# Performance work log

Measured on AMD Instinct MI355X. Metric: run time of the kernel, lower is better.

The kernel has to match this reference:

```python
import jax, jax.numpy as jnp
import numpy as np

BS, L, D, K, G, E = 512, 128, 512, 30, 8, 2048
H = E // 2  # MLP hidden = embed_dim // 2


def setup_inputs():
    key = jax.random.key(0)
    ks = jax.random.split(key, 8)
    features = jax.random.normal(ks[0], (BS, L, D), jnp.float32)
    atten = jax.random.uniform(ks[1], (BS, L, L), jnp.float32)
    rng = np.random.default_rng(0)
    lens = rng.integers(34, L - 1, size=BS)          # caption lengths (>= 34 so lengths-2 > K)
    toks = rng.integers(1, 1000, size=(BS, L))
    pos = np.arange(L)[None, :]
    text = np.where(pos < lens[:, None], toks, 0)    # zero padding
    text[np.arange(BS), lens - 1] = 49407            # eos = max token id -> argmax finds it
    text = jnp.asarray(text, jnp.int32)
    pid = jnp.asarray(np.repeat(np.arange(BS // G), G), jnp.int32)  # 64 groups of size G=8
    dlp_w = jax.random.normal(ks[2], (G, D), jnp.float32)           # weights['weight_8']
    dlp_b = jnp.zeros((G,), jnp.float32)                            # biases['bias_8']
    dlp_lw = jax.random.normal(ks[3], (K * G, E), jnp.float32) * 0.05  # linears['linear_8']
    dlp_lb = jnp.zeros((E,), jnp.float32)
    mlp_w1 = jax.random.normal(ks[4], (D, H), jnp.float32) * 0.04
    mlp_b1 = jnp.zeros((H,), jnp.float32)
    bn_g = jnp.ones((H,), jnp.float32)
    bn_b = jnp.zeros((H,), jnp.float32)
    mlp_w2 = jax.random.normal(ks[5], (H, E), jnp.float32) * 0.03
    mlp_b2 = jnp.zeros((E,), jnp.float32)
    return dict(features=features, atten=atten, text=text, pid=pid,
                dlp_w=dlp_w, dlp_b=dlp_b, dlp_lw=dlp_lw, dlp_lb=dlp_lb,
                mlp_w1=mlp_w1, mlp_b1=mlp_b1, bn_g=bn_g, bn_b=bn_b,
                mlp_w2=mlp_w2, mlp_b2=mlp_b2)


def _l2norm(x, eps=1e-8):
    return x / (jnp.sqrt(jnp.sum(x * x, axis=-1, keepdims=True)) + eps)


def _groups_from_pid(pid_np):
    # replicates the pid_dist==0 grouping + dedup-by-member-set, preserving first-seen order
    groups, order = {}, []
    for i, p in enumerate(pid_np.tolist()):
        if p not in groups:
            groups[p] = []
            order.append(p)
        groups[p].append(i)
    return [groups[p] for p in order]


def reference(features, atten, text, pid, dlp_w, dlp_b, dlp_lw, dlp_lb,
              mlp_w1, mlp_b1, bn_g, bn_b, mlp_w2, mlp_b2):
    bs = features.shape[0]
    b = jnp.arange(bs)
    mask = (text != 0).astype(features.dtype)                  # [bs, L]
    lengths = mask.sum(1) - 2.0                                # [bs]
    eos = jnp.argmax(text, axis=-1)                            # [bs]
    att = atten.at[b, :, eos].set(-1.0).at[:, :, 0].set(-1.0)
    row = att[b, eos, :] * mask                                # [bs, L]
    idx = jax.lax.top_k(row, K)[1]                             # [bs, K] topk token indices
    feats = jnp.take_along_axis(features, idx[:, :, None], axis=1)  # [bs, K, D]

    # pid-based dynamic grouping (host-side; pid is an index input, static)
    glists = _groups_from_pid(np.asarray(pid))
    assert {len(g) for g in glists} == {G}, 'expert params provided for group size G only'
    gi = np.asarray(glists)                                    # [ng, G]
    xg = feats[gi].reshape(gi.shape[0], G * K, D)              # concat group members: [ng, G*K, D]
    # F.linear(x, W[G,D], b).T  ->  [ng, G, G*K]
    h = jnp.einsum('ntd,gd->ngt', xg, dlp_w) + dlp_b[None, :, None]
    yg = h @ dlp_lw + dlp_lb                                   # linear_G: [ng, G, E]
    # scatter-combine each member's row back to its batch position
    new_base = jnp.zeros((bs, E), feats.dtype).at[gi.reshape(-1)].set(yg.reshape(-1, E))
    new_base = _l2norm(new_base)

    # MLP (Linear -> BatchNorm1d(train stats) -> ReLU -> Linear) on l2-normed gathered feats
    x = _l2norm(feats).reshape(bs * K, D) @ mlp_w1 + mlp_b1
    mu, var = x.mean(0), x.var(0)
    x = jax.nn.relu((x - mu) / jnp.sqrt(var + 1e-5) * bn_g + bn_b)
    x = (x @ mlp_w2 + mlp_b2).reshape(bs, K, E)

    # maxk_pool1d_var with pool k=1: per-channel max over first min(length, K) rows
    lens = jnp.minimum(lengths, K).astype(jnp.int32)
    valid = jnp.arange(K)[None, :] < lens[:, None]             # [bs, K]
    pooled = jnp.max(jnp.where(valid[:, :, None], x, -jnp.inf), axis=1)  # [bs, E]
    return (pooled + new_base).astype(jnp.float32)
```

## Files before the change

kernel.cpp:

```cpp
#include <hip/hip_runtime.h>
#include <hip/hip_bf16.h>

#define BS 512
#define LL 128
#define DD 512
#define KK 30
#define GG 8
#define EE 2048
#define HH 1024
#define NROWS (BS*KK)
#define NG (BS/GG)

typedef __attribute__((ext_vector_type(8))) short bf16x8;
typedef __attribute__((ext_vector_type(4))) float f32x4;
typedef __attribute__((address_space(1))) const unsigned int gu32;
typedef __attribute__((address_space(3))) unsigned int lu32;

__device__ __forceinline__ unsigned short f2bf(float f){
  unsigned int x = __float_as_uint(f);
  x = (x + 0x7FFFu + ((x >> 16) & 1u)) >> 16;
  return (unsigned short)x;
}
__device__ __forceinline__ float bf2f(unsigned short u){
  return __uint_as_float(((unsigned int)u) << 16);
}
__device__ __forceinline__ unsigned fkey(float f){
  unsigned b = __float_as_uint(f);
  return (b & 0x80000000u) ? ~b : (b | 0x80000000u);
}
__device__ __forceinline__ float fdec(unsigned k){
  unsigned b = (k & 0x80000000u) ? (k & 0x7FFFFFFFu) : ~k;
  return __uint_as_float(b);
}

__global__ __launch_bounds__(64) void k_prep(const float* __restrict__ atten,
                                             const int* __restrict__ text,
                                             int* __restrict__ idx,
                                             int* __restrict__ lensk){
  const int b = blockIdx.x;
  const int lane = threadIdx.x;
  const int t0 = text[b*LL + lane];
  const int t1 = text[b*LL + 64 + lane];

  int v, vi;
  if(t1 > t0){ v = t1; vi = lane + 64; } else { v = t0; vi = lane; }
#pragma unroll
  for(int off = 32; off; off >>= 1){
    const int ov = __shfl_xor(v, off), oi = __shfl_xor(vi, off);
    if(ov > v || (ov == v && oi < vi)){ v = ov; vi = oi; }
  }
  const int eos = vi;

  const unsigned long long mb0 = __ballot(t0 != 0), mb1 = __ballot(t1 != 0);
  if(lane == 0) lensk[b] = min(__popcll(mb0) + __popcll(mb1) - 2, KK);

  const float a0 = atten[(size_t)b*LL*LL + (size_t)eos*LL + lane];
  const float a1 = atten[(size_t)b*LL*LL + (size_t)eos*LL + 64 + lane];
  float r0 = (t0 == 0) ? 0.f : ((lane == 0 || lane == eos) ? -1.f : a0);
  float r1 = (t1 == 0) ? 0.f : ((lane + 64 == eos) ? -1.f : a1);

  for(int k = 0; k < KK; k++){
    float mv; int mi;
    if(r1 > r0){ mv = r1; mi = lane + 64; } else { mv = r0; mi = lane; }
#pragma unroll
    for(int off = 32; off; off >>= 1){
      const float ov = __shfl_xor(mv, off); const int oi = __shfl_xor(mi, off);
      if(ov > mv || (ov == mv && oi < mi)){ mv = ov; mi = oi; }
    }
    if(lane == 0) idx[b*KK + k] = mi;
    if(mi == lane)      r0 = -3.f;
    if(mi == lane + 64) r1 = -3.f;
  }
}

__global__ __launch_bounds__(128) void k_gather(const float* __restrict__ features,
                                                const float* __restrict__ dlp_w,
                                                const float* __restrict__ dlp_b,
                                                const int* __restrict__ idx,
                                                unsigned short* __restrict__ nfeats,
                                                float* __restrict__ hval){
  const int r = blockIdx.x;
  const int b = r / KK;
  const int t = threadIdx.x;
  const int l = idx[r];

  const float4 v = ((const float4*)features)[((size_t)b*LL + l)*(DD/4) + t];
  float ss = v.x*v.x + v.y*v.y + v.z*v.z + v.w*v.w;
  float hg[GG];
#pragma unroll
  for(int g = 0; g < GG; g++){
    const float4 w = ((const float4*)dlp_w)[g*(DD/4) + t];
    hg[g] = v.x*w.x + v.y*w.y + v.z*w.z + v.w*w.w;
  }
#pragma unroll
  for(int off = 32; off > 0; off >>= 1){
    ss += __shfl_down(ss, off);
#pragma unroll
    for(int g = 0; g < GG; g++) hg[g] += __shfl_down(hg[g], off);
  }
  __shared__ float red[2][9];
  __shared__ float s_rn;
  const int wave = t >> 6, lane = t & 63;
  if(lane == 0){
    red[wave][0] = ss;
#pragma unroll
    for(int g = 0; g < GG; g++) red[wave][1+g] = hg[g];
  }
  __syncthreads();
  if(t == 0) s_rn = 1.0f / (sqrtf(red[0][0] + red[1][0]) + 1e-8f);
  if(t < GG) hval[(size_t)r*GG + t] = red[0][1+t] + red[1][1+t] + dlp_b[t];
  __syncthreads();
  const float rn = s_rn;
  ushort4 u;
  u.x = f2bf(v.x*rn); u.y = f2bf(v.y*rn); u.z = f2bf(v.z*rn); u.w = f2bf(v.w*rn);
  ((ushort4*)nfeats)[(size_t)r*(DD/4) + t] = u;
}

__global__ __launch_bounds__(256) void k_dlp(const float* __restrict__ hval,
                                             const float* __restrict__ dlp_lw,
                                             const float* __restrict__ dlp_lb,
                                             unsigned short* __restrict__ nbbf){
  const int et = blockIdx.x;
  const int n  = blockIdx.y;
  const int tid = threadIdx.x;
  __shared__ float hs[GG][GG*KK];
  for(int i = tid; i < GG*GG*KK; i += 256){
    const int g = i / (GG*KK), tt = i % (GG*KK);
    const int m = tt / KK, kq = tt % KK;
    hs[g][tt] = hval[(size_t)(((n*GG + m)*KK) + kq)*GG + g];
  }
  __syncthreads();
  const int h = tid >> 7, c = tid & 127;
  const int e = et*128 + c;
  float acc[4] = {0.f, 0.f, 0.f, 0.f};
#pragma unroll 4
  for(int k = 0; k < GG*KK; k++){
    const float w = dlp_lw[(size_t)k*EE + e];
#pragma unroll
    for(int rr = 0; rr < 4; rr++) acc[rr] += hs[h*4 + rr][k] * w;
  }
  const float lb = dlp_lb[e];
#pragma unroll
  for(int rr = 0; rr < 4; rr++)
    nbbf[(size_t)(n*GG + h*4 + rr)*EE + e] = f2bf(acc[rr] + lb);
}

__global__ __launch_bounds__(256) void k_l2nb(unsigned short* __restrict__ nbbf){
  const int b = blockIdx.x, t = threadIdx.x;
  uint4* p = (uint4*)(nbbf + (size_t)b*EE);
  uint4 u = p[t];
  unsigned short* us = (unsigned short*)&u;
  float f[8]; float ss = 0.f;
#pragma unroll
  for(int j = 0; j < 8; j++){ f[j] = bf2f(us[j]); ss += f[j]*f[j]; }
#pragma unroll
  for(int off = 32; off > 0; off >>= 1) ss += __shfl_down(ss, off);
  __shared__ float red[4];
  __shared__ float s_rn;
  if((t & 63) == 0) red[t >> 6] = ss;
  __syncthreads();
  if(t == 0) s_rn = 1.0f / (sqrtf(red[0] + red[1] + red[2] + red[3]) + 1e-8f);
  __syncthreads();
  const float rn = s_rn;
#pragma unroll
  for(int j = 0; j < 8; j++) us[j] = f2bf(f[j]*rn);
  p[t] = u;
}

__global__ __launch_bounds__(256) void k_wcvt(const float* __restrict__ src,
                                              unsigned short* __restrict__ dst,
                                              int Kd, int Nd){
  __shared__ float tile[32][33];
  const int n0 = blockIdx.x*32, k0 = blockIdx.y*32;
  const int r = threadIdx.x >> 3, c4 = (threadIdx.x & 7)*4;
  const float4 v = *(const float4*)(src + (size_t)(k0 + r)*Nd + n0 + c4);
  tile[r][c4+0] = v.x; tile[r][c4+1] = v.y; tile[r][c4+2] = v.z; tile[r][c4+3] = v.w;
  __syncthreads();
  ushort4 u;
  u.x = f2bf(tile[c4+0][r]); u.y = f2bf(tile[c4+1][r]);
  u.z = f2bf(tile[c4+2][r]); u.w = f2bf(tile[c4+3][r]);
  *(ushort4*)(dst + (size_t)(n0 + r)*Kd + k0 + c4) = u;
}

template<int KD, int ND, bool POOL, bool STATS, int NBX>
__global__ __launch_bounds__(512, 2) void k_mgemm(const unsigned short* __restrict__ A,
                                                  const unsigned short* __restrict__ Bt,
                                                  const float* __restrict__ bias,
                                                  unsigned short* __restrict__ obf,
                                                  const int* __restrict__ lensk,
                                                  unsigned* __restrict__ pkey,
                                                  float* __restrict__ psum,
                                                  float* __restrict__ psq){
  __shared__ short S[2][2][256*64];
  const int tid  = threadIdx.x;
  const int wave = tid >> 6, lane = tid & 63;
  const int wr = wave >> 2, wc = wave & 3;
  const int lrow = lane & 15, kg = lane >> 4;

  const int nwg = gridDim.x, cpx = nwg >> 3;
  const int bid = (blockIdx.x & 7)*cpx + (blockIdx.x >> 3);
  const int bx = bid % NBX, by = bid / NBX;
  const int m0 = by*256, n0 = bx*256;

  const unsigned short* Ab = A  + (size_t)m0*KD;
  const unsigned short* Bb = Bt + (size_t)n0*KD;

#define STG_A(tt, p, c) { \
  const int i_ = tid + (c)*512; const int r_ = i_ >> 3; \
  const int g_ = (i_ & 7) ^ (r_ & 7); \
  __builtin_amdgcn_global_load_lds((gu32*)(Ab + (size_t)r_*KD + (tt)*64 + g_*8), \
                                   (lu32*)(&S[p][0][i_*8]), 16, 0, 0); }
#define STG_B(tt, p, c) { \
  const int i_ = tid + (c)*512; const int r_ = i_ >> 3; \
  const int g_ = (i_ & 7) ^ (r_ & 7); \
  __builtin_amdgcn_global_load_lds((gu32*)(Bb + (size_t)r_*KD + (tt)*64 + g_*8), \
                                   (lu32*)(&S[p][1][i_*8]), 16, 0, 0); }

  f32x4 acc[8][4] = {};
  const int NT = KD/64;

  STG_A(0, 0, 0) STG_A(0, 0, 2)
  STG_B(0, 0, 0) STG_B(0, 0, 1) STG_B(0, 0, 2) STG_B(0, 0, 3)
  STG_A(0, 0, 1) STG_A(0, 0, 3)

  const int arow = wr*128 + lrow;
  const int brow = wc*64  + lrow;
  const int gx0 = ((0*4 + kg) ^ (lrow & 7))*8;
  const int gx1 = ((1*4 + kg) ^ (lrow & 7))*8;

  for(int t = 0; t < NT; t++){
    const int p = t & 1;
    const short* Abuf = &S[p][0][0];
    const short* Bbuf = &S[p][1][0];

    asm volatile("s_waitcnt vmcnt(2)" ::: "memory");
    __builtin_amdgcn_s_barrier();
    asm volatile("" ::: "memory");
    if(t + 1 < NT){
      STG_A(t+1, p^1, 0) STG_A(t+1, p^1, 2)
      STG_B(t+1, p^1, 0) STG_B(t+1, p^1, 1) STG_B(t+1, p^1, 2) STG_B(t+1, p^1, 3)
    }
    bf16x8 bg0[4], bg1[4], af[4];
#pragma unroll
    for(int n = 0; n < 4; n++){
      bg0[n] = *(const bf16x8*)(Bbuf + (brow + n*16)*64 + gx0);
      bg1[n] = *(const bf16x8*)(Bbuf + (brow + n*16)*64 + gx1);
    }
#pragma unroll
    for(int m = 0; m < 4; m++)
      af[m] = *(const bf16x8*)(Abuf + (arow + m*16)*64 + gx0);
    __builtin_amdgcn_s_setprio(1);
#pragma unroll
    for(int m = 0; m < 4; m++)
#pragma unroll
      for(int n = 0; n < 4; n++)
        acc[m][n] = __builtin_amdgcn_mfma_f32_16x16x32_bf16(af[m], bg0[n], acc[m][n], 0, 0, 0);
#pragma unroll
    for(int m = 0; m < 4; m++)
      af[m] = *(const bf16x8*)(Abuf + (arow + m*16)*64 + gx1);
#pragma unroll
    for(int m = 0; m < 4; m++)
#pragma unroll
      for(int n = 0; n < 4; n++)
        acc[m][n] = __builtin_amdgcn_mfma_f32_16x16x32_bf16(af[m], bg1[n], acc[m][n], 0, 0, 0);
    __builtin_amdgcn_s_setprio(0);

    if(t + 1 < NT) asm volatile("s_waitcnt vmcnt(6)" ::: "memory");
    else           asm volatile("s_waitcnt vmcnt(0)" ::: "memory");
    __builtin_amdgcn_s_barrier();
    asm volatile("" ::: "memory");
    if(t + 1 < NT){ STG_A(t+1, p^1, 1) STG_A(t+1, p^1, 3) }
#pragma unroll
    for(int m = 0; m < 4; m++)
      af[m] = *(const bf16x8*)(Abuf + (arow + 64 + m*16)*64 + gx0);
    __builtin_amdgcn_s_setprio(1);
#pragma unroll
    for(int m = 0; m < 4; m++)
#pragma unroll
      for(int n = 0; n < 4; n++)
        acc[4+m][n] = __builtin_amdgcn_mfma_f32_16x16x32_bf16(af[m], bg0[n], acc[4+m][n], 0, 0, 0);
#pragma unroll
    for(int m = 0; m < 4; m++)
      af[m] = *(const bf16x8*)(Abuf + (arow + 64 + m*16)*64 + gx1);
#pragma unroll
    for(int m = 0; m < 4; m++)
#pragma unroll
      for(int n = 0; n < 4; n++)
        acc[4+m][n] = __builtin_amdgcn_mfma_f32_16x16x32_bf16(af[m], bg1[n], acc[4+m][n], 0, 0, 0);
    __builtin_amdgcn_s_setprio(0);
  }
#undef STG_A
#undef STG_B

  if constexpr (!POOL){
    const int colb = n0 + wc*64 + lrow;
#pragma unroll
    for(int n = 0; n < 4; n++){
      const float bb = bias[colb + n*16];
      if constexpr (STATS){
        float sv = 0.f, qv = 0.f;
#pragma unroll
        for(int m = 0; m < 8; m++)
#pragma unroll
          for(int r = 0; r < 4; r++){
            const float v = acc[m][n][r] + bb; sv += v; qv += v*v;
          }
        sv += __shfl_xor(sv, 16); sv += __shfl_xor(sv, 32);
        qv += __shfl_xor(qv, 16); qv += __shfl_xor(qv, 32);
        if(lane < 16){
          psum[(size_t)(by*2 + wr)*ND + colb + n*16] = sv;
          psq [(size_t)(by*2 + wr)*ND + colb + n*16] = qv;
        }
      }
#pragma unroll
      for(int m = 0; m < 8; m++){
        const int row = m0 + wr*128 + m*16 + kg*4;
#pragma unroll
        for(int r = 0; r < 4; r++)
          obf[(size_t)(row + r)*ND + colb + n*16] = f2bf(acc[m][n][r] + bb);
      }
    }
  } else {
    __syncthreads();
    unsigned* pool = (unsigned*)&S[0][0][0];
    const int b0 = m0 / KK;
    const int b1 = (m0 + 255) / KK;
    const int nseg = b1 - b0 + 1;
    for(int i = tid; i < nseg*256; i += 512) pool[i] = 0x007FFFFFu;
    __syncthreads();
    const int lcol = wc*64 + lrow;
    {
      int cur_b = -1;
      float mx[4];
#pragma unroll
      for(int m = 0; m < 8; m++){
#pragma unroll
        for(int r = 0; r < 4; r++){
          const int row = m0 + wr*128 + m*16 + kg*4 + r;
          const int bt = row / KK;
          const int rr = row - bt*KK;
          if(bt != cur_b){
            if(cur_b >= 0){
#pragma unroll
              for(int n = 0; n < 4; n++)
                atomicMax(&pool[(cur_b - b0)*256 + lcol + n*16], fkey(mx[n]));
            }
            cur_b = bt;
#pragma unroll
            for(int n = 0; n < 4; n++) mx[n] = -INFINITY;
          }
          if(rr < lensk[bt]){
#pragma unroll
            for(int n = 0; n < 4; n++) mx[n] = fmaxf(mx[n], acc[m][n][r]);
          }
        }
      }
#pragma unroll
      for(int n = 0; n < 4; n++)
        atomicMax(&pool[(cur_b - b0)*256 + lcol + n*16], fkey(mx[n]));
    }
    __syncthreads();
    for(int e = tid; e < nseg*256; e += 512){
      const int seg = e >> 8, col = e & 255;
      atomicMax(&pkey[(size_t)(b0 + seg)*ND + n0 + col], pool[e]);
    }
  }
}

__global__ __launch_bounds__(256) void k_bnfin(const float* __restrict__ psum,
                                               const float* __restrict__ psq,
                                               const float* __restrict__ bn_g,
                                               const float* __restrict__ bn_b,
                                               float* __restrict__ sc,
                                               float* __restrict__ sh){
  const int c = blockIdx.x*256 + threadIdx.x;
  float s = 0.f, q = 0.f;
  for(int i = 0; i < 120; i++){ s += psum[(size_t)i*HH + c]; q += psq[(size_t)i*HH + c]; }
  const float mu  = s * (1.0f/NROWS);
  const float var = q * (1.0f/NROWS) - mu*mu;
  const float sv  = bn_g[c] / sqrtf(var + 1e-5f);
  sc[c] = sv;
  sh[c] = bn_b[c] - mu*sv;
}

__global__ __launch_bounds__(256) void k_bnrelu(unsigned short* __restrict__ x1,
                                                const float* __restrict__ sc,
                                                const float* __restrict__ sh,
                                                unsigned* __restrict__ pkey){
  const size_t i = (size_t)blockIdx.x*256 + threadIdx.x;
  const int c0 = (int)((i*8) & (HH-1));
  uint4 u = ((uint4*)x1)[i];
  unsigned short* us = (unsigned short*)&u;
  const float4 s0 = *(const float4*)(sc + c0), s1 = *(const float4*)(sc + c0 + 4);
  const float4 h0 = *(const float4*)(sh + c0), h1 = *(const float4*)(sh + c0 + 4);
  const float scv[8] = {s0.x,s0.y,s0.z,s0.w,s1.x,s1.y,s1.z,s1.w};
  const float shv[8] = {h0.x,h0.y,h0.z,h0.w,h1.x,h1.y,h1.z,h1.w};
#pragma unroll
  for(int j = 0; j < 8; j++)
    us[j] = f2bf(fmaxf(bf2f(us[j])*scv[j] + shv[j], 0.f));
  ((uint4*)x1)[i] = u;
  if(blockIdx.x < 1024)
    ((uint4*)pkey)[blockIdx.x*256 + threadIdx.x] =
        make_uint4(0x007FFFFFu, 0x007FFFFFu, 0x007FFFFFu, 0x007FFFFFu);
}

__global__ __launch_bounds__(256) void k_final(const unsigned* __restrict__ pkey,
                                               const float* __restrict__ b2,
                                               const unsigned short* __restrict__ nbbf,
                                               float* __restrict__ out){
  const size_t i = (size_t)blockIdx.x*256 + threadIdx.x;
  const int c0 = (int)((i*4) & (EE-1));
  const uint4 k = ((const uint4*)pkey)[i];
  const ushort4 nb4 = ((const ushort4*)nbbf)[i];
  const float4 b = *(const float4*)(b2 + c0);
  float4 o;
  o.x = fdec(k.x) + b.x + bf2f(nb4.x);
  o.y = fdec(k.y) + b.y + bf2f(nb4.y);
  o.z = fdec(k.z) + b.z + bf2f(nb4.z);
  o.w = fdec(k.w) + b.w + bf2f(nb4.w);
  ((float4*)out)[i] = o;
}

extern "C" void kernel_launch(void* const* d_in, const int* in_sizes, int n_in,
                              void* d_out, int out_size, void* d_ws, size_t ws_size,
                              hipStream_t stream){
  const float* features = (const float*)d_in[0];
  const float* atten    = (const float*)d_in[1];
  const int*   text     = (const int*)  d_in[2];
  const float* dlp_w    = (const float*)d_in[4];
  const float* dlp_b    = (const float*)d_in[5];
  const float* dlp_lw   = (const float*)d_in[6];
  const float* dlp_lb   = (const float*)d_in[7];
  const float* w1       = (const float*)d_in[8];
  const float* b1       = (const float*)d_in[9];
  const float* bn_g     = (const float*)d_in[10];
  const float* bn_b     = (const float*)d_in[11];
  const float* w2       = (const float*)d_in[12];
  const float* b2       = (const float*)d_in[13];
  float* out = (float*)d_out;

  char* ws = (char*)d_ws;
  float*          psum   = (float*)(ws + 0);
  float*          psq    = (float*)(ws + 983040);
  unsigned short* w1t    = (unsigned short*)(ws + 1966080);
  float*          hval   = (float*)(ws + 3014656);
  int*            idx    = (int*)(ws + 3506176);
  unsigned*       pkey   = (unsigned*)(ws + 0);
  int*            lensk  = (int*)(ws + 4194304);
  float*          sc     = (float*)(ws + 4196352);
  float*          sh     = (float*)(ws + 4200448);
  unsigned short* nfeats = (unsigned short*)(ws + 4204544);
  unsigned short* w2t    = (unsigned short*)(ws + 4204544);
  unsigned short* x1     = (unsigned short*)(ws + 19933184);
  unsigned short* nbbf   = (unsigned short*)(ws + 51390464);

  k_wcvt<<<dim3(HH/32, DD/32), 256, 0, stream>>>(w1, w1t, DD, HH);
  k_prep<<<BS, 64, 0, stream>>>(atten, text, idx, lensk);
  k_gather<<<NROWS, 128, 0, stream>>>(features, dlp_w, dlp_b, idx, nfeats, hval);
  k_dlp<<<dim3(16, NG), 256, 0, stream>>>(hval, dlp_lw, dlp_lb, nbbf);
  k_l2nb<<<BS, 256, 0, stream>>>(nbbf);
  k_mgemm<DD, HH, false, true, HH/256><<<(HH/256)*(NROWS/256), 512, 0, stream>>>(
      nfeats, w1t, b1, x1, nullptr, nullptr, psum, psq);
  k_wcvt<<<dim3(EE/32, HH/32), 256, 0, stream>>>(w2, w2t, HH, EE);
  k_bnfin<<<4, 256, 0, stream>>>(psum, psq, bn_g, bn_b, sc, sh);
  k_bnrelu<<<(NROWS*HH/8)/256, 256, 0, stream>>>(x1, sc, sh, pkey);
  k_mgemm<HH, EE, true, false, EE/256><<<(EE/256)*(NROWS/256), 512, 0, stream>>>(
      x1, w2t, nullptr, nullptr, lensk, pkey, nullptr, nullptr);
  k_final<<<(BS*EE/4)/256, 256, 0, stream>>>(pkey, b2, nbbf, out);
}
```

Measured before the change: 209.8 us.

## Restructure GEMM main loop into four-phase barrier-synchronized pipeline with peeled tail

Reorganizes the 256x256 bf16 MFMA GEMM inner loop into four sub-phases per k-tile. Each phase interleaves LDS reads, global-to-LDS prefetch of the next tile, and a 4x4 MFMA block, with explicit barriers, lgkmcnt waits and sched_barrier fences. This is meant to let waves stagger so memory issue overlaps MFMA execution, and to cut register pressure by holding one B fragment set instead of two. The last iteration is peeled to drop the per-iteration conditionals. The cost is more barriers per tile, which may add sync overhead.

```diff
diff --git a/kernel.cpp b/kernel.cpp
--- a/kernel.cpp
+++ b/kernel.cpp
@@ -216,81 +216,99 @@
   __builtin_amdgcn_global_load_lds((gu32*)(Bb + (size_t)r_*KD + (tt)*64 + g_*8), \
                                    (lu32*)(&S[p][1][i_*8]), 16, 0, 0); }
 
+#define DSR_B(gx)  _Pragma("unroll") for(int n = 0; n < 4; n++) \
+    bg[n] = *(const bf16x8*)(Bbuf + (brow + n*16)*64 + (gx));
+#define DSR_AL(gx) _Pragma("unroll") for(int m = 0; m < 4; m++) \
+    af[m] = *(const bf16x8*)(Abuf + (arow + m*16)*64 + (gx));
+#define DSR_AH(gx) _Pragma("unroll") for(int m = 0; m < 4; m++) \
+    af[m] = *(const bf16x8*)(Abuf + (arow + 64 + m*16)*64 + (gx));
+#define FENCE asm volatile("" ::: "memory")
+#define BARR  do{ FENCE; __builtin_amdgcn_s_barrier(); FENCE; }while(0)
+#define LGK0  do{ asm volatile("s_waitcnt lgkmcnt(0)" ::: "memory"); \
+                  __builtin_amdgcn_sched_barrier(0); }while(0)
+#define VMW(n) asm volatile("s_waitcnt vmcnt(" #n ")" ::: "memory")
+#define MFMA_L do{ __builtin_amdgcn_s_setprio(1); \
+  _Pragma("unroll") for(int m = 0; m < 4; m++) \
+  _Pragma("unroll") for(int n = 0; n < 4; n++) \
+    acc[m][n] = __builtin_amdgcn_mfma_f32_16x16x32_bf16(af[m], bg[n], acc[m][n], 0, 0, 0); \
+  __builtin_amdgcn_s_setprio(0); }while(0)
+#define MFMA_H do{ __builtin_amdgcn_s_setprio(1); \
+  _Pragma("unroll") for(int m = 0; m < 4; m++) \
+  _Pragma("unroll") for(int n = 0; n < 4; n++) \
+    acc[4+m][n] = __builtin_amdgcn_mfma_f32_16x16x32_bf16(af[m], bg[n], acc[4+m][n], 0, 0, 0); \
+  __builtin_amdgcn_s_setprio(0); }while(0)
+
   f32x4 acc[8][4] = {};
   const int NT = KD/64;
+
+  const int arow = wr*128 + lrow;
+  const int brow = wc*64  + lrow;
+  const int gx0 = (kg       ^ (lrow & 7))*8;
+  const int gx1 = ((4 + kg) ^ (lrow & 7))*8;
 
   STG_A(0, 0, 0) STG_A(0, 0, 2)
   STG_B(0, 0, 0) STG_B(0, 0, 1) STG_B(0, 0, 2) STG_B(0, 0, 3)
   STG_A(0, 0, 1) STG_A(0, 0, 3)
-
-  const int arow = wr*128 + lrow;
-  const int brow = wc*64  + lrow;
-  const int gx0 = ((0*4 + kg) ^ (lrow & 7))*8;
-  const int gx1 = ((1*4 + kg) ^ (lrow & 7))*8;
-
-  for(int t = 0; t < NT; t++){
-    const int p = t & 1;
+  VMW(2); BARR;
+
+#pragma unroll 1
+  for(int t = 0; t < NT-1; t++){
+    const int p = t & 1, q = p ^ 1;
     const short* Abuf = &S[p][0][0];
     const short* Bbuf = &S[p][1][0];
-
-    asm volatile("s_waitcnt vmcnt(2)" ::: "memory");
-    __builtin_amdgcn_s_barrier();
-    asm volatile("" ::: "memory");
-    if(t + 1 < NT){
-      STG_A(t+1, p^1, 0) STG_A(t+1, p^1, 2)
-      STG_B(t+1, p^1, 0) STG_B(t+1, p^1, 1) STG_B(t+1, p^1, 2) STG_B(t+1, p^1, 3)
-    }
-    bf16x8 bg0[4], bg1[4], af[4];
-#pragma unroll
-    for(int n = 0; n < 4; n++){
-      bg0[n] = *(const bf16x8*)(Bbuf + (brow + n*16)*64 + gx0);
-      bg1[n] = *(const bf16x8*)(Bbuf + (brow + n*16)*64 + gx1);
-    }
-#pragma unroll
-    for(int m = 0; m < 4; m++)
-      af[m] = *(const bf16x8*)(Abuf + (arow + m*16)*64 + gx0);
-    __builtin_amdgcn_s_setprio(1);
-#pragma unroll
-    for(int m = 0; m < 4; m++)
-#pragma unroll
-      for(int n = 0; n < 4; n++)
-        acc[m][n] = __builtin_amdgcn_mfma_f32_16x16x32_bf16(af[m], bg0[n], acc[m][n], 0, 0, 0);
-#pragma unroll
-    for(int m = 0; m < 4; m++)
-      af[m] = *(const bf16x8*)(Abuf + (arow + m*16)*64 + gx1);
-#pragma unroll
-    for(int m = 0; m < 4; m++)
-#pragma unroll
-      for(int n = 0; n < 4; n++)
-        acc[m][n] = __builtin_amdgcn_mfma_f32_16x16x32_bf16(af[m], bg1[n], acc[m][n], 0, 0, 0);
-    __builtin_amdgcn_s_setprio(0);
-
-    if(t + 1 < NT) asm volatile("s_waitcnt vmcnt(6)" ::: "memory");
-    else           asm volatile("s_waitcnt vmcnt(0)" ::: "memory");
-    __builtin_amdgcn_s_barrier();
-    asm volatile("" ::: "memory");
-    if(t + 1 < NT){ STG_A(t+1, p^1, 1) STG_A(t+1, p^1, 3) }
-#pragma unroll
-    for(int m = 0; m < 4; m++)
-      af[m] = *(const bf16x8*)(Abuf + (arow + 64 + m*16)*64 + gx0);
-    __builtin_amdgcn_s_setprio(1);
-#pragma unroll
-    for(int m = 0; m < 4; m++)
-#pragma unroll
-      for(int n = 0; n < 4; n++)
-        acc[4+m][n] = __builtin_amdgcn_mfma_f32_16x16x32_bf16(af[m], bg0[n], acc[4+m][n], 0, 0, 0);
-#pragma unroll
-    for(int m = 0; m < 4; m++)
-      af[m] = *(const bf16x8*)(Abuf + (arow + 64 + m*16)*64 + gx1);
-#pragma unroll
-    for(int m = 0; m < 4; m++)
-#pragma unroll
-      for(int n = 0; n < 4; n++)
-        acc[4+m][n] = __builtin_amdgcn_mfma_f32_16x16x32_bf16(af[m], bg1[n], acc[4+m][n], 0, 0, 0);
-    __builtin_amdgcn_s_setprio(0);
+    bf16x8 bg[4], af[4];
+    DSR_B(gx0); DSR_AL(gx0);
+    STG_A(t+1, q, 0) STG_A(t+1, q, 2)
+    VMW(2);
+    BARR; LGK0;
+    MFMA_L;
+    BARR;
+    DSR_AH(gx0);
+    STG_B(t+1, q, 0) STG_B(t+1, q, 1)
+    BARR; LGK0;
+    MFMA_H;
+    BARR;
+    DSR_B(gx1); DSR_AL(gx1);
+    STG_B(t+1, q, 2) STG_B(t+1, q, 3)
+    BARR; LGK0;
+    MFMA_L;
+    BARR;
+    DSR_AH(gx1);
+    STG_A(t+1, q, 1) STG_A(t+1, q, 3)
+    VMW(2);
+    BARR; LGK0;
+    MFMA_H;
+    BARR;
+  }
+  {
+    const int p = (NT-1) & 1;
+    const short* Abuf = &S[p][0][0];
+    const short* Bbuf = &S[p][1][0];
+    bf16x8 bg[4], af[4];
+    DSR_B(gx0); DSR_AL(gx0);
+    VMW(0);
+    BARR; LGK0;
+    MFMA_L;
+    BARR;
+    DSR_AH(gx0);
+    BARR; LGK0;
+    MFMA_H;
+    BARR;
+    DSR_B(gx1); DSR_AL(gx1);
+    BARR; LGK0;
+    MFMA_L;
+    BARR;
+    DSR_AH(gx1);
+    LGK0;
+    MFMA_H;
   }
 #undef STG_A
 #undef STG_B
+#undef DSR_B
+#undef DSR_AL
+#undef DSR_AH
+#undef MFMA_L
+#undef MFMA_H
 
   if constexpr (!POOL){
     const int colb = n0 + wc*64 + lrow;
```

Measured after the change: 213.0 us. Within noise of the previous version (+1.5%).
